# Optimization experiments

Hardware: AMD Instinct MI355X
Metric: run time of the kernel (lower is better)

Reference implementation:

```python
import jax, jax.numpy as jnp
import numpy as np

B, T, H, NPRED = 256, 512, 512, 128


def setup_inputs() -> dict:
    key = jax.random.key(0)
    ks = jax.random.split(key, 16)
    s = 1.0 / np.sqrt(H)
    u = lambda k, shape: jax.random.uniform(k, shape, jnp.float32, -s, s)
    return {
        "x": jax.random.normal(ks[0], (B, T), jnp.float32),
        # PyTorch LSTM params, gate order (i, f, g, o); bias = b_ih + b_hh fused
        "enc_Wih0": u(ks[1], (4 * H, 1)),
        "enc_Whh0": u(ks[2], (4 * H, H)),
        "enc_b0": u(ks[3], (4 * H,)),
        "enc_Wih1": u(ks[4], (4 * H, H)),
        "enc_Whh1": u(ks[5], (4 * H, H)),
        "enc_b1": u(ks[6], (4 * H,)),
        "dec_Wih0": u(ks[7], (4 * H, 1)),
        "dec_Whh0": u(ks[8], (4 * H, H)),
        "dec_b0": u(ks[9], (4 * H,)),
        "dec_Wih1": u(ks[10], (4 * H, H)),
        "dec_Whh1": u(ks[11], (4 * H, H)),
        "dec_b1": u(ks[12], (4 * H,)),
        "lin_W": u(ks[13], (H,)),
        "lin_b": u(ks[14], ()),
        "num_predictions": NPRED,
    }


def _cell(xp, h, c, Whh):
    # xp: x @ Wih.T + b (precomputed), shape [B, 4H]
    g = xp + h @ Whh.T
    i, f, gg, o = jnp.split(g, 4, axis=-1)
    c2 = jax.nn.sigmoid(f) * c + jax.nn.sigmoid(i) * jnp.tanh(gg)
    h2 = jax.nn.sigmoid(o) * jnp.tanh(c2)
    return h2, c2


def _lstm_layer(xs, Wih, Whh, b):
    # xs: [B, T, D] -> outputs [B, T, H], final (h, c) each [B, H]
    xp = jnp.einsum('btd,gd->btg', xs, Wih) + b  # input projection for all steps
    Bb = xs.shape[0]
    h0 = jnp.zeros((Bb, Whh.shape[1]), xs.dtype)
    c0 = jnp.zeros_like(h0)

    def step(carry, xt):
        h, c = carry
        h2, c2 = _cell(xt, h, c, Whh)
        return (h2, c2), h2

    (hT, cT), hs = jax.lax.scan(step, (h0, c0), jnp.swapaxes(xp, 0, 1))
    return jnp.swapaxes(hs, 0, 1), hT, cT


def reference(x, enc_Wih0, enc_Whh0, enc_b0, enc_Wih1, enc_Whh1, enc_b1,
              dec_Wih0, dec_Whh0, dec_b0, dec_Wih1, dec_Whh1, dec_b1,
              lin_W, lin_b, num_predictions):
    # Encoder: 2-layer LSTM over the full sequence (encode() feeds [B,T,1] once)
    h_l0, e_h0, e_c0 = _lstm_layer(x[:, :, None], enc_Wih0, enc_Whh0, enc_b0)
    _, e_h1, e_c1 = _lstm_layer(h_l0, enc_Wih1, enc_Whh1, enc_b1)

    def dec_step(carry, _):
        h0, c0, h1, c1, prev = carry
        xp0 = prev[:, None] @ dec_Wih0.T + dec_b0  # [B, 4H]
        h0n, c0n = _cell(xp0, h0, c0, dec_Whh0)
        xp1 = h0n @ dec_Wih1.T + dec_b1
        h1n, c1n = _cell(xp1, h1, c1, dec_Whh1)
        pred = h1n @ lin_W + lin_b  # [B]
        return (h0n, c0n, h1n, c1n, pred), pred

    carry0 = (e_h0, e_c0, e_h1, e_c1, x[:, -1])
    _, preds = jax.lax.scan(dec_step, carry0, None, length=num_predictions)
    return jnp.swapaxes(preds, 0, 1)  # [B, num_predictions]
```

## Files before the change

### kernel.cpp

```cpp
#include <hip/hip_runtime.h>

#define Hh 512
#define Bb 256
#define Tt 512
#define NPR 128
#define BH (Bb*Hh)
#define WN (4*Hh*Hh)
#define LDSB (131072 + 256)

typedef __attribute__((ext_vector_type(8))) short bf8;
typedef __attribute__((ext_vector_type(4))) float f4;
typedef __attribute__((ext_vector_type(4))) unsigned u4;

#define MF(A,B,C) C = __builtin_amdgcn_mfma_f32_16x16x32_bf16(A,B,C,0,0,0)
#define ALD(p)    __hip_atomic_load((p),  __ATOMIC_RELAXED, __HIP_MEMORY_SCOPE_AGENT)
#define AST(p,v)  __hip_atomic_store((p), (v), __ATOMIC_RELAXED, __HIP_MEMORY_SCOPE_AGENT)

__device__ __forceinline__ void ld16(u4& d, const u4* p) {
  asm volatile("global_load_dwordx4 %0, %1, off sc0 sc1" : "=&v"(d) : "v"(p));
}
__device__ __forceinline__ void st16(u4* p, u4 d) {
  asm volatile("global_store_dwordx4 %0, %1, off sc0 sc1" :: "v"(p), "v"(d) : "memory");
}
__device__ __forceinline__ bf8 asbf8(u4 v) {
  union { u4 u; bf8 b; } c; c.u = v; return c.b;
}
#define VW16 { asm volatile("s_waitcnt vmcnt(16)" ::: "memory"); __builtin_amdgcn_sched_barrier(0); }
#define VW0  { asm volatile("s_waitcnt vmcnt(0)"  ::: "memory"); __builtin_amdgcn_sched_barrier(0); }

__device__ __forceinline__ unsigned short f2bf(float x) {
  unsigned u = __float_as_uint(x);
  return (unsigned short)((u + 0x7FFFu + ((u >> 16) & 1u)) >> 16);
}
__device__ __forceinline__ float bf2f(unsigned short h) {
  return __uint_as_float((unsigned)h << 16);
}

__device__ __forceinline__ float sigm(float x) {
  return __builtin_amdgcn_rcpf(1.f + __expf(-x));
}
__device__ __forceinline__ float tanh_f(float x) {
  x = fminf(15.f, fmaxf(-15.f, x));
  const float e = __expf(2.f * x);
  return (e - 1.f) * __builtin_amdgcn_rcpf(e + 1.f);
}

__device__ __forceinline__ u4 pack8(unsigned short v, int lane) {
  unsigned x = v;
  unsigned p1 = (unsigned)__shfl_xor((int)x, 1, 64);
  unsigned u  = (lane & 1) ? ((p1 & 0xFFFFu) | (x << 16)) : ((x & 0xFFFFu) | (p1 << 16));
  unsigned p2 = (unsigned)__shfl_xor((int)u, 2, 64);
  unsigned d0 = (lane & 2) ? p2 : u;
  unsigned d1 = (lane & 2) ? u  : p2;
  unsigned q0 = (unsigned)__shfl_xor((int)d0, 4, 64);
  unsigned q1 = (unsigned)__shfl_xor((int)d1, 4, 64);
  u4 r;
  if (lane & 4) { r[0] = q0; r[1] = q1; r[2] = d0; r[3] = d1; }
  else          { r[0] = d0; r[1] = d1; r[2] = q0; r[3] = q1; }
  return r;
}

struct KP {
  const float *x, *eb0, *eb1, *db0, *db1, *eWih0, *dWih0, *linW, *linb;
  const unsigned short *eWhh0h,*eWhh0l,*eWih1h,*eWih1l,*eWhh1h,*eWhh1l;
  const unsigned short *dWhh0h,*dWhh0l,*dWih1h,*dWih1l,*dWhh1h,*dWhh1l;
  u4 *h0h0,*h0h1,*h0l0,*h0l1,*h1h0,*h1h1,*h1l0,*h1l1;
  float *c0,*c1,*pred,*out;
  unsigned *bar;
};

__device__ void gsync(unsigned* bar, unsigned rnd) {
  asm volatile("s_waitcnt vmcnt(0)" ::: "memory");
  __syncthreads();
  if (threadIdx.x == 0) {
    unsigned* ctr  = bar;
    unsigned* flag = bar + 64;
    const unsigned a = __hip_atomic_fetch_add(ctr, 1u, __ATOMIC_RELAXED, __HIP_MEMORY_SCOPE_AGENT);
    if (a == rnd*256u + 255u) AST(flag, rnd + 1u);
    while (ALD(flag) <= rnd) __builtin_amdgcn_s_sleep(1);
  }
  __syncthreads();
  asm volatile("" ::: "memory");
}

__device__ void stageA_w(const unsigned short* Wh, const unsigned short* Wl, int j0, char* L) {
  const int t = threadIdx.x;
  const int r = t >> 3, q = t & 7;
  const int n = (r >> 4)*Hh + j0 + (r & 15);
  const unsigned short* gh = Wh + (size_t)n*Hh;
  const unsigned short* gl = Wl + (size_t)n*Hh;
  char* rowp = L + r*1024;
  #pragma unroll
  for (int u = 0; u < 8; ++u) {
    const int s = q*8 + u;
    const int so = (s ^ (r & 7)) * 16;
    *(uint4*)(rowp + so)         = *(const uint4*)(gh + s*8);
    *(uint4*)(rowp + 65536 + so) = *(const uint4*)(gl + s*8);
  }
  __syncthreads();
}
__device__ void stageB_w(const unsigned short* Wh, const unsigned short* Wl, int j0, char* slab) {
  const int t = threadIdx.x;
  const int r = t >> 4, q = t & 15;
  const int n = (r >> 3)*Hh + j0 + (r & 7);
  const unsigned short* gh = Wh + (size_t)n*Hh;
  const unsigned short* gl = Wl + (size_t)n*Hh;
  char* rowp = slab + r*1024;
  #pragma unroll
  for (int u = 0; u < 4; ++u) {
    const int s = q*4 + u;
    const int so = (s ^ (r & 7)) * 16;
    *(uint4*)(rowp + so)         = *(const uint4*)(gh + s*8);
    *(uint4*)(rowp + 32768 + so) = *(const uint4*)(gl + s*8);
  }
  __syncthreads();
}

__device__ __forceinline__ void stepA(const KP& kp, const char* L, float* sS,
    int m0, int j0, int jg,
    const u4* Ah, const u4* Al,
    const float* sW, const float* bias, float* cst,
    u4* Ho, u4* Lo, int smode, int sarg)
{
  const int tid = threadIdx.x;
  if (smode == 0) {
    if (tid < 64) sS[tid] = kp.x[(size_t)(m0 + tid)*Tt + sarg];
  } else if (tid < 256) {
    const int bl = tid >> 2, part = tid & 3;
    const int b = m0 + bl;
    float a = 0.f;
    #pragma unroll
    for (int u = 0; u < 16; ++u)
      a += ALD(&kp.pred[(part*16 + u)*Bb + b]);
    a += __shfl_xor(a, 1, 64);
    a += __shfl_xor(a, 2, 64);
    const float s = a + kp.linb[0];
    if (part == 0) {
      sS[bl] = s;
      if (jg == 0 && sarg >= 1) kp.out[(size_t)b*NPR + (sarg - 1)] = s;
    }
  }
  __syncthreads();

  const int wv = tid >> 6;
  if (wv >= 4) return;
  const int lane = tid & 63;
  const int r15 = lane & 15, kg = lane >> 4;
  const int bb = m0 + wv*16 + r15;
  const u4* pAh = Ah + kg*256 + bb;
  const u4* pAl = Al + kg*256 + bb;
  f4 acc[4];
  #pragma unroll
  for (int g = 0; g < 4; ++g) acc[g] = (f4){0.f,0.f,0.f,0.f};
  const int swz = r15 & 7;

  u4 vh[16], vl[16];
  #pragma unroll
  for (int q = 0; q < 16; ++q) {
    ld16(vh[q], pAh + q*1024);
    ld16(vl[q], pAl + q*1024);
  }
  VW16;
  #pragma unroll
  for (int q = 0; q < 8; ++q) {
    const int so = ((q*4 + kg) ^ swz) * 16;
    const bf8 a_h = asbf8(vh[q]), a_l = asbf8(vl[q]);
    #pragma unroll
    for (int g = 0; g < 4; ++g) {
      const int ro = (g*16 + r15)*1024 + so;
      const bf8 w_h = *(const bf8*)(L + ro);
      const bf8 w_l = *(const bf8*)(L + 65536 + ro);
      MF(a_h, w_h, acc[g]); MF(a_l, w_h, acc[g]); MF(a_h, w_l, acc[g]);
    }
  }
  VW0;
  #pragma unroll
  for (int q = 8; q < 16; ++q) {
    const int so = ((q*4 + kg) ^ swz) * 16;
    const bf8 a_h = asbf8(vh[q]), a_l = asbf8(vl[q]);
    #pragma unroll
    for (int g = 0; g < 4; ++g) {
      const int ro = (g*16 + r15)*1024 + so;
      const bf8 w_h = *(const bf8*)(L + ro);
      const bf8 w_l = *(const bf8*)(L + 65536 + ro);
      MF(a_h, w_h, acc[g]); MF(a_l, w_h, acc[g]); MF(a_h, w_l, acc[g]);
    }
  }

  const int j = j0 + r15;
  const float sw0 = sW[j], sw1 = sW[Hh+j], sw2 = sW[2*Hh+j], sw3 = sW[3*Hh+j];
  const float bi = bias[j], bfv = bias[Hh+j], bgv = bias[2*Hh+j], bo = bias[3*Hh+j];
  const int kcA = jg*2 + (r15 >> 3);
  #pragma unroll
  for (int r = 0; r < 4; ++r) {
    const int bloc = wv*16 + kg*4 + r;
    const float sv = sS[bloc];
    const size_t idx = (size_t)(m0 + bloc)*Hh + j;
    const float gi = acc[0][r] + bi  + sv*sw0;
    const float gf = acc[1][r] + bfv + sv*sw1;
    const float gg = acc[2][r] + bgv + sv*sw2;
    const float go = acc[3][r] + bo  + sv*sw3;
    const float c2 = sigm(gf) * cst[idx] + sigm(gi) * tanh_f(gg);
    const float h2 = sigm(go) * tanh_f(c2);
    cst[idx] = c2;
    const unsigned short hh2 = f2bf(h2);
    const unsigned short ll2 = f2bf(h2 - bf2f(hh2));
    const u4 ph = pack8(hh2, lane);
    const u4 pl = pack8(ll2, lane);
    const int slot = kcA*256 + (m0 + wv*16 + kg*4 + r);
    if ((r15 & 7) == 0) { st16(Ho + slot, ph); st16(Lo + slot, pl); }
  }
}

__device__ __forceinline__ void stepB_gemm(const char* Wslab,
    const u4* Ah, const u4* Al, int m0, f4* acc)
{
  const int tid = threadIdx.x, wv = tid >> 6, lane = tid & 63;
  const int r15 = lane & 15, kg = lane >> 4;
  const int swz = r15 & 7;
  const char* Wh = Wslab;
  const char* Wl = Wslab + 32768;
  const int bb = m0 + wv*16 + r15;
  const u4* pAh = Ah + kg*256 + bb;
  const u4* pAl = Al + kg*256 + bb;
  u4 vh[16], vl[16];
  #pragma unroll
  for (int q = 0; q < 16; ++q) {
    ld16(vh[q], pAh + q*1024);
    ld16(vl[q], pAl + q*1024);
  }
  VW16;
  #pragma unroll
  for (int q = 0; q < 8; ++q) {
    const int so = ((q*4 + kg) ^ swz) * 16;
    const bf8 a_h = asbf8(vh[q]), a_l = asbf8(vl[q]);
    const bf8 w0h = *(const bf8*)(Wh + r15*1024 + so);
    const bf8 w1h = *(const bf8*)(Wh + (16 + r15)*1024 + so);
    const bf8 w0l = *(const bf8*)(Wl + r15*1024 + so);
    const bf8 w1l = *(const bf8*)(Wl + (16 + r15)*1024 + so);
    MF(a_h, w0h, acc[0]); MF(a_l, w0h, acc[0]); MF(a_h, w0l, acc[0]);
    MF(a_h, w1h, acc[1]); MF(a_l, w1h, acc[1]); MF(a_h, w1l, acc[1]);
  }
  VW0;
  #pragma unroll
  for (int q = 8; q < 16; ++q) {
    const int so = ((q*4 + kg) ^ swz) * 16;
    const bf8 a_h = asbf8(vh[q]), a_l = asbf8(vl[q]);
    const bf8 w0h = *(const bf8*)(Wh + r15*1024 + so);
    const bf8 w1h = *(const bf8*)(Wh + (16 + r15)*1024 + so);
    const bf8 w0l = *(const bf8*)(Wl + r15*1024 + so);
    const bf8 w1l = *(const bf8*)(Wl + (16 + r15)*1024 + so);
    MF(a_h, w0h, acc[0]); MF(a_l, w0h, acc[0]); MF(a_h, w0l, acc[0]);
    MF(a_h, w1h, acc[1]); MF(a_l, w1h, acc[1]); MF(a_h, w1l, acc[1]);
  }
}

__device__ __forceinline__ void stepB_fin(const KP& kp, int m0, int j0, int jg,
    f4* acc, const float* bias, float* cst, u4* Ho, u4* Lo, int doPred)
{
  const int tid = threadIdx.x, wv = tid >> 6, lane = tid & 63;
  const int r15 = lane & 15, kg = lane >> 4;
  float og0[4], og1[4];
  #pragma unroll
  for (int c = 0; c < 4; ++c) {
    og0[c] = __shfl_xor(acc[0][c], 8, 64);
    og1[c] = __shfl_xor(acc[1][c], 8, 64);
  }
  const bool own = (r15 < 8);
  const int j = j0 + (r15 & 7);
  const float bi = bias[j], bfv = bias[Hh+j], bgv = bias[2*Hh+j], bo = bias[3*Hh+j];
  float hs[4];
  #pragma unroll
  for (int r = 0; r < 4; ++r) {
    const int bl = wv*16 + kg*4 + r;
    const size_t idx = (size_t)(m0 + bl)*Hh + j;
    const float gi = acc[0][r] + bi;
    const float gf = og0[r]    + bfv;
    const float gg = acc[1][r] + bgv;
    const float go = og1[r]    + bo;
    const float cold = own ? cst[idx] : 0.f;
    const float c2 = sigm(gf) * cold + sigm(gi) * tanh_f(gg);
    const float h2 = sigm(go) * tanh_f(c2);
    if (own) cst[idx] = c2;
    const unsigned short hh2 = f2bf(h2);
    const unsigned short ll2 = f2bf(h2 - bf2f(hh2));
    const u4 ph = pack8(hh2, lane);
    const u4 pl = pack8(ll2, lane);
    const int slot = jg*256 + (m0 + wv*16 + kg*4 + r);
    if (r15 == 0) { st16(Ho + slot, ph); st16(Lo + slot, pl); }
    hs[r] = h2;
  }
  if (doPred) {
    const float lw = kp.linW[j];
    #pragma unroll
    for (int r = 0; r < 4; ++r) {
      float p = hs[r] * lw;
      p += __shfl_xor(p, 1, 64);
      p += __shfl_xor(p, 2, 64);
      p += __shfl_xor(p, 4, 64);
      if (r15 == 0)
        AST(&kp.pred[jg*Bb + (m0 + wv*16 + kg*4 + r)], p);
    }
  }
}

#define PH0(p) ((p) ? kp.h0h1 : kp.h0h0)
#define PL0(p) ((p) ? kp.h0l1 : kp.h0l0)
#define PH1(p) ((p) ? kp.h1h1 : kp.h1h0)
#define PL1(p) ((p) ? kp.h1l1 : kp.h1l0)

__global__ __launch_bounds__(512) void lstm_persist(KP kp) {
  extern __shared__ char L[];
  float* sS = (float*)(L + 131072);
  const int blk = blockIdx.x;
  const bool roleA = blk < 128;
  int m0, j0, jg;
  if (roleA) { jg = blk >> 2; m0 = (blk & 3) * 64; j0 = jg * 16; }
  else { const int b2 = blk - 128; jg = b2 >> 1; m0 = (b2 & 1) * 128; j0 = jg * 8; }

  if (roleA) stageA_w(kp.eWhh0h, kp.eWhh0l, j0, L);
  else { stageB_w(kp.eWih1h, kp.eWih1l, j0, L); stageB_w(kp.eWhh1h, kp.eWhh1l, j0, L + 65536); }

  unsigned rnd = 0;

  for (int s = 0; s <= Tt; ++s) {
    if (roleA) {
      if (s < Tt)
        stepA(kp, L, sS, m0, j0, jg, PH0(s&1), PL0(s&1), kp.eWih0, kp.eb0,
              kp.c0, PH0((s+1)&1), PL0((s+1)&1), 0, s);
    } else {
      if (s >= 1) {
        f4 acc[2]; acc[0] = acc[1] = (f4){0.f,0.f,0.f,0.f};
        stepB_gemm(L,         PH0(s&1),     PL0(s&1),     m0, acc);
        stepB_gemm(L + 65536, PH1((s-1)&1), PL1((s-1)&1), m0, acc);
        stepB_fin(kp, m0, j0, jg, acc, kp.eb1, kp.c1, PH1(s&1), PL1(s&1), 0);
      }
    }
    gsync(kp.bar, rnd++);
  }

  if (roleA) stageA_w(kp.dWhh0h, kp.dWhh0l, j0, L);
  else { stageB_w(kp.dWih1h, kp.dWih1l, j0, L); stageB_w(kp.dWhh1h, kp.dWhh1l, j0, L + 65536); }

  for (int i = 0; i < NPR; ++i) {
    f4 acc[2]; acc[0] = acc[1] = (f4){0.f,0.f,0.f,0.f};
    if (roleA) {
      if (i == 0)
        stepA(kp, L, sS, m0, j0, jg, PH0(0), PL0(0), kp.dWih0, kp.db0,
              kp.c0, PH0(1), PL0(1), 0, Tt - 1);
      else
        stepA(kp, L, sS, m0, j0, jg, PH0(i&1), PL0(i&1), kp.dWih0, kp.db0,
              kp.c0, PH0((i+1)&1), PL0((i+1)&1), 1, i);
    } else {
      stepB_gemm(L + 65536, PH1(i&1), PL1(i&1), m0, acc);
    }
    gsync(kp.bar, rnd++);
    if (!roleA) {
      stepB_gemm(L, PH0((i+1)&1), PL0((i+1)&1), m0, acc);
      stepB_fin(kp, m0, j0, jg, acc, kp.db1, kp.c1, PH1((i+1)&1), PL1((i+1)&1), 1);
    }
    gsync(kp.bar, rnd++);
  }

  if (roleA && jg == 0 && threadIdx.x < 256) {
    const int tid = threadIdx.x, bl = tid >> 2, part = tid & 3, b = m0 + bl;
    float a = 0.f;
    #pragma unroll
    for (int u = 0; u < 16; ++u) a += ALD(&kp.pred[(part*16 + u)*Bb + b]);
    a += __shfl_xor(a, 1, 64);
    a += __shfl_xor(a, 2, 64);
    if (part == 0) kp.out[(size_t)b*NPR + 127] = a + kp.linb[0];
  }
}

__global__ __launch_bounds__(256) void conv_w(const float* __restrict__ src,
                                              unsigned short* __restrict__ hi,
                                              unsigned short* __restrict__ lo) {
  const int i = (blockIdx.x * 256 + threadIdx.x) * 4;
  const float4 v = *(const float4*)(src + i);
  const unsigned short h0 = f2bf(v.x), h1 = f2bf(v.y), h2 = f2bf(v.z), h3 = f2bf(v.w);
  ushort4 hv; hv.x = h0; hv.y = h1; hv.z = h2; hv.w = h3;
  ushort4 lv;
  lv.x = f2bf(v.x - bf2f(h0)); lv.y = f2bf(v.y - bf2f(h1));
  lv.z = f2bf(v.z - bf2f(h2)); lv.w = f2bf(v.w - bf2f(h3));
  *(ushort4*)(hi + i) = hv;
  *(ushort4*)(lo + i) = lv;
}

extern "C" void kernel_launch(void* const* d_in, const int* in_sizes, int n_in,
                              void* d_out, int out_size, void* d_ws, size_t ws_size,
                              hipStream_t stream) {
  const float* x     = (const float*)d_in[0];
  const float* eWih0 = (const float*)d_in[1];
  const float* eWhh0 = (const float*)d_in[2];
  const float* eb0   = (const float*)d_in[3];
  const float* eWih1 = (const float*)d_in[4];
  const float* eWhh1 = (const float*)d_in[5];
  const float* eb1   = (const float*)d_in[6];
  const float* dWih0 = (const float*)d_in[7];
  const float* dWhh0 = (const float*)d_in[8];
  const float* db0   = (const float*)d_in[9];
  const float* dWih1 = (const float*)d_in[10];
  const float* dWhh1 = (const float*)d_in[11];
  const float* db1   = (const float*)d_in[12];
  const float* linW  = (const float*)d_in[13];
  const float* linb  = (const float*)d_in[14];
  float* out = (float*)d_out;

  unsigned short* wb = (unsigned short*)d_ws;
  unsigned short* W[12];
  for (int k = 0; k < 12; ++k) W[k] = wb + (size_t)k*WN;
  unsigned short* sb = wb + (size_t)12*WN;
  float* cb   = (float*)(sb + (size_t)8*BH);
  float* c0   = cb;
  float* c1   = cb + BH;
  float* pred = cb + 2*(size_t)BH;
  unsigned* bar = (unsigned*)(pred + 64*Bb);

  (void)hipMemsetAsync(sb + 0*(size_t)BH, 0, (size_t)BH*2, stream);
  (void)hipMemsetAsync(sb + 2*(size_t)BH, 0, (size_t)BH*2, stream);
  (void)hipMemsetAsync(sb + 4*(size_t)BH, 0, (size_t)BH*2, stream);
  (void)hipMemsetAsync(sb + 6*(size_t)BH, 0, (size_t)BH*2, stream);
  (void)hipMemsetAsync(c0, 0, (size_t)BH*4, stream);
  (void)hipMemsetAsync(c1, 0, (size_t)BH*4, stream);
  (void)hipMemsetAsync(bar, 0, 4096, stream);

  conv_w<<<1024, 256, 0, stream>>>(eWhh0, W[0], W[1]);
  conv_w<<<1024, 256, 0, stream>>>(eWih1, W[2], W[3]);
  conv_w<<<1024, 256, 0, stream>>>(eWhh1, W[4], W[5]);
  conv_w<<<1024, 256, 0, stream>>>(dWhh0, W[6], W[7]);
  conv_w<<<1024, 256, 0, stream>>>(dWih1, W[8], W[9]);
  conv_w<<<1024, 256, 0, stream>>>(dWhh1, W[10], W[11]);

  KP kp;
  kp.x = x; kp.eb0 = eb0; kp.eb1 = eb1; kp.db0 = db0; kp.db1 = db1;
  kp.eWih0 = eWih0; kp.dWih0 = dWih0; kp.linW = linW; kp.linb = linb;
  kp.eWhh0h = W[0]; kp.eWhh0l = W[1];
  kp.eWih1h = W[2]; kp.eWih1l = W[3];
  kp.eWhh1h = W[4]; kp.eWhh1l = W[5];
  kp.dWhh0h = W[6]; kp.dWhh0l = W[7];
  kp.dWih1h = W[8]; kp.dWih1l = W[9];
  kp.dWhh1h = W[10]; kp.dWhh1l = W[11];
  kp.h0h0 = (u4*)(sb + 0*(size_t)BH); kp.h0h1 = (u4*)(sb + 1*(size_t)BH);
  kp.h0l0 = (u4*)(sb + 2*(size_t)BH); kp.h0l1 = (u4*)(sb + 3*(size_t)BH);
  kp.h1h0 = (u4*)(sb + 4*(size_t)BH); kp.h1h1 = (u4*)(sb + 5*(size_t)BH);
  kp.h1l0 = (u4*)(sb + 6*(size_t)BH); kp.h1l1 = (u4*)(sb + 7*(size_t)BH);
  kp.c0 = c0; kp.c1 = c1; kp.pred = pred; kp.out = out; kp.bar = bar;

  (void)hipFuncSetAttribute((const void*)lstm_persist,
                            hipFuncAttributeMaxDynamicSharedMemorySize, LDSB);
  void* kargs[] = { (void*)&kp };
  hipError_t rc = hipLaunchCooperativeKernel((const void*)lstm_persist, dim3(256), dim3(512),
                                             kargs, LDSB, stream);
  if (rc != hipSuccess) {
    lstm_persist<<<dim3(256), dim3(512), LDSB, stream>>>(kp);
  }
  (void)in_sizes; (void)n_in; (void)out_size; (void)ws_size;
}
```

Measured before the change: 9.454 ms.

## Keep LSTM cell state in LDS and use cached loads with per-sync invalidation

Cell state c for both layers is now held in each block's shared memory instead of global arrays, since every block owns a fixed batch/hidden tile across all steps. This removes global c reads and writes and their memsets. Hidden-state loads drop the sc0 sc1 cache-bypass bits. To keep cross-block visibility correct, the grid barrier now issues a buffer_inv, and output writes become atomic stores. The risk is stale data if the invalidation or the ownership assumptions do not fully hold.

```diff
diff --git a/kernel.cpp b/kernel.cpp
--- a/kernel.cpp
+++ b/kernel.cpp
@@ -6,7 +6,7 @@
 #define NPR 128
 #define BH (Bb*Hh)
 #define WN (4*Hh*Hh)
-#define LDSB (131072 + 256)
+#define LDSB (131072 + 256 + 4608)
 
 typedef __attribute__((ext_vector_type(8))) short bf8;
 typedef __attribute__((ext_vector_type(4))) float f4;
@@ -17,7 +17,7 @@
 #define AST(p,v)  __hip_atomic_store((p), (v), __ATOMIC_RELAXED, __HIP_MEMORY_SCOPE_AGENT)
 
 __device__ __forceinline__ void ld16(u4& d, const u4* p) {
-  asm volatile("global_load_dwordx4 %0, %1, off sc0 sc1" : "=&v"(d) : "v"(p));
+  asm volatile("global_load_dwordx4 %0, %1, off" : "=&v"(d) : "v"(p));
 }
 __device__ __forceinline__ void st16(u4* p, u4 d) {
   asm volatile("global_store_dwordx4 %0, %1, off sc0 sc1" :: "v"(p), "v"(d) : "memory");
@@ -80,7 +80,7 @@
     while (ALD(flag) <= rnd) __builtin_amdgcn_s_sleep(1);
   }
   __syncthreads();
-  asm volatile("" ::: "memory");
+  asm volatile("buffer_inv sc0 sc1\n\ts_waitcnt vmcnt(0)" ::: "memory");
 }
 
 __device__ void stageA_w(const unsigned short* Wh, const unsigned short* Wl, int j0, char* L) {
@@ -116,10 +116,10 @@
   __syncthreads();
 }
 
-__device__ __forceinline__ void stepA(const KP& kp, const char* L, float* sS,
+__device__ __forceinline__ void stepA(const KP& kp, const char* L, float* sS, float* cS,
     int m0, int j0, int jg,
     const u4* Ah, const u4* Al,
-    const float* sW, const float* bias, float* cst,
+    const float* sW, const float* bias,
     u4* Ho, u4* Lo, int smode, int sarg)
 {
   const int tid = threadIdx.x;
@@ -137,7 +137,7 @@
     const float s = a + kp.linb[0];
     if (part == 0) {
       sS[bl] = s;
-      if (jg == 0 && sarg >= 1) kp.out[(size_t)b*NPR + (sarg - 1)] = s;
+      if (jg == 0 && sarg >= 1) AST(&kp.out[(size_t)b*NPR + (sarg - 1)], s);
     }
   }
   __syncthreads();
@@ -200,15 +200,16 @@
     const float gf = acc[1][r] + bfv + sv*sw1;
     const float gg = acc[2][r] + bgv + sv*sw2;
     const float go = acc[3][r] + bo  + sv*sw3;
-    const float c2 = sigm(gf) * cst[idx] + sigm(gi) * tanh_f(gg);
+    const float c2 = sigm(gf) * cS[bloc*17 + r15] + sigm(gi) * tanh_f(gg);
     const float h2 = sigm(go) * tanh_f(c2);
-    cst[idx] = c2;
+    cS[bloc*17 + r15] = c2;
     const unsigned short hh2 = f2bf(h2);
     const unsigned short ll2 = f2bf(h2 - bf2f(hh2));
     const u4 ph = pack8(hh2, lane);
     const u4 pl = pack8(ll2, lane);
     const int slot = kcA*256 + (m0 + wv*16 + kg*4 + r);
     if ((r15 & 7) == 0) { st16(Ho + slot, ph); st16(Lo + slot, pl); }
+    (void)idx;
   }
 }
 
@@ -255,8 +256,8 @@
   }
 }
 
-__device__ __forceinline__ void stepB_fin(const KP& kp, int m0, int j0, int jg,
-    f4* acc, const float* bias, float* cst, u4* Ho, u4* Lo, int doPred)
+__device__ __forceinline__ void stepB_fin(const KP& kp, float* cS, int m0, int j0, int jg,
+    f4* acc, const float* bias, u4* Ho, u4* Lo, int doPred)
 {
   const int tid = threadIdx.x, wv = tid >> 6, lane = tid & 63;
   const int r15 = lane & 15, kg = lane >> 4;
@@ -273,15 +274,14 @@
   #pragma unroll
   for (int r = 0; r < 4; ++r) {
     const int bl = wv*16 + kg*4 + r;
-    const size_t idx = (size_t)(m0 + bl)*Hh + j;
     const float gi = acc[0][r] + bi;
     const float gf = og0[r]    + bfv;
     const float gg = acc[1][r] + bgv;
     const float go = og1[r]    + bo;
-    const float cold = own ? cst[idx] : 0.f;
+    const float cold = own ? cS[bl*9 + (r15 & 7)] : 0.f;
     const float c2 = sigm(gf) * cold + sigm(gi) * tanh_f(gg);
     const float h2 = sigm(go) * tanh_f(c2);
-    if (own) cst[idx] = c2;
+    if (own) cS[bl*9 + (r15 & 7)] = c2;
     const unsigned short hh2 = f2bf(h2);
     const unsigned short ll2 = f2bf(h2 - bf2f(hh2));
     const u4 ph = pack8(hh2, lane);
@@ -312,12 +312,15 @@
 __global__ __launch_bounds__(512) void lstm_persist(KP kp) {
   extern __shared__ char L[];
   float* sS = (float*)(L + 131072);
+  float* cS = (float*)(L + 131072 + 256);
   const int blk = blockIdx.x;
   const bool roleA = blk < 128;
   int m0, j0, jg;
   if (roleA) { jg = blk >> 2; m0 = (blk & 3) * 64; j0 = jg * 16; }
   else { const int b2 = blk - 128; jg = b2 >> 1; m0 = (b2 & 1) * 128; j0 = jg * 8; }
 
+  for (int i = threadIdx.x; i < 1152; i += 512) cS[i] = 0.f;
+
   if (roleA) stageA_w(kp.eWhh0h, kp.eWhh0l, j0, L);
   else { stageB_w(kp.eWih1h, kp.eWih1l, j0, L); stageB_w(kp.eWhh1h, kp.eWhh1l, j0, L + 65536); }
 
@@ -326,14 +329,14 @@
   for (int s = 0; s <= Tt; ++s) {
     if (roleA) {
       if (s < Tt)
-        stepA(kp, L, sS, m0, j0, jg, PH0(s&1), PL0(s&1), kp.eWih0, kp.eb0,
-              kp.c0, PH0((s+1)&1), PL0((s+1)&1), 0, s);
+        stepA(kp, L, sS, cS, m0, j0, jg, PH0(s&1), PL0(s&1), kp.eWih0, kp.eb0,
+              PH0((s+1)&1), PL0((s+1)&1), 0, s);
     } else {
       if (s >= 1) {
         f4 acc[2]; acc[0] = acc[1] = (f4){0.f,0.f,0.f,0.f};
         stepB_gemm(L,         PH0(s&1),     PL0(s&1),     m0, acc);
         stepB_gemm(L + 65536, PH1((s-1)&1), PL1((s-1)&1), m0, acc);
-        stepB_fin(kp, m0, j0, jg, acc, kp.eb1, kp.c1, PH1(s&1), PL1(s&1), 0);
+        stepB_fin(kp, cS, m0, j0, jg, acc, kp.eb1, PH1(s&1), PL1(s&1), 0);
       }
     }
     gsync(kp.bar, rnd++);
@@ -346,18 +349,18 @@
     f4 acc[2]; acc[0] = acc[1] = (f4){0.f,0.f,0.f,0.f};
     if (roleA) {
       if (i == 0)
-        stepA(kp, L, sS, m0, j0, jg, PH0(0), PL0(0), kp.dWih0, kp.db0,
-              kp.c0, PH0(1), PL0(1), 0, Tt - 1);
+        stepA(kp, L, sS, cS, m0, j0, jg, PH0(0), PL0(0), kp.dWih0, kp.db0,
+              PH0(1), PL0(1), 0, Tt - 1);
       else
-        stepA(kp, L, sS, m0, j0, jg, PH0(i&1), PL0(i&1), kp.dWih0, kp.db0,
-              kp.c0, PH0((i+1)&1), PL0((i+1)&1), 1, i);
+        stepA(kp, L, sS, cS, m0, j0, jg, PH0(i&1), PL0(i&1), kp.dWih0, kp.db0,
+              PH0((i+1)&1), PL0((i+1)&1), 1, i);
     } else {
       stepB_gemm(L + 65536, PH1(i&1), PL1(i&1), m0, acc);
     }
     gsync(kp.bar, rnd++);
     if (!roleA) {
       stepB_gemm(L, PH0((i+1)&1), PL0((i+1)&1), m0, acc);
-      stepB_fin(kp, m0, j0, jg, acc, kp.db1, kp.c1, PH1((i+1)&1), PL1((i+1)&1), 1);
+      stepB_fin(kp, cS, m0, j0, jg, acc, kp.db1, PH1((i+1)&1), PL1((i+1)&1), 1);
     }
     gsync(kp.bar, rnd++);
   }
@@ -369,7 +372,7 @@
     for (int u = 0; u < 16; ++u) a += ALD(&kp.pred[(part*16 + u)*Bb + b]);
     a += __shfl_xor(a, 1, 64);
     a += __shfl_xor(a, 2, 64);
-    if (part == 0) kp.out[(size_t)b*NPR + 127] = a + kp.linb[0];
+    if (part == 0) AST(&kp.out[(size_t)b*NPR + 127], a + kp.linb[0]);
   }
 }
 
@@ -412,8 +415,6 @@
   for (int k = 0; k < 12; ++k) W[k] = wb + (size_t)k*WN;
   unsigned short* sb = wb + (size_t)12*WN;
   float* cb   = (float*)(sb + (size_t)8*BH);
-  float* c0   = cb;
-  float* c1   = cb + BH;
   float* pred = cb + 2*(size_t)BH;
   unsigned* bar = (unsigned*)(pred + 64*Bb);
 
@@ -421,8 +422,6 @@
   (void)hipMemsetAsync(sb + 2*(size_t)BH, 0, (size_t)BH*2, stream);
   (void)hipMemsetAsync(sb + 4*(size_t)BH, 0, (size_t)BH*2, stream);
   (void)hipMemsetAsync(sb + 6*(size_t)BH, 0, (size_t)BH*2, stream);
-  (void)hipMemsetAsync(c0, 0, (size_t)BH*4, stream);
-  (void)hipMemsetAsync(c1, 0, (size_t)BH*4, stream);
   (void)hipMemsetAsync(bar, 0, 4096, stream);
 
   conv_w<<<1024, 256, 0, stream>>>(eWhh0, W[0], W[1]);
@@ -445,7 +444,7 @@
   kp.h0l0 = (u4*)(sb + 2*(size_t)BH); kp.h0l1 = (u4*)(sb + 3*(size_t)BH);
   kp.h1h0 = (u4*)(sb + 4*(size_t)BH); kp.h1h1 = (u4*)(sb + 5*(size_t)BH);
   kp.h1l0 = (u4*)(sb + 6*(size_t)BH); kp.h1l1 = (u4*)(sb + 7*(size_t)BH);
-  kp.c0 = c0; kp.c1 = c1; kp.pred = pred; kp.out = out; kp.bar = bar;
+  kp.c0 = cb; kp.c1 = cb + BH; kp.pred = pred; kp.out = out; kp.bar = bar;
 
   (void)hipFuncSetAttribute((const void*)lstm_persist,
                             hipFuncAttributeMaxDynamicSharedMemorySize, LDSB);
```

Result: slower. 20.43 ms (+116.0%).
